# Kernel optimization log

Measured on AMD Instinct MI355X. Metric: run time of the kernel, lower is better.

## Reference

```python
import jax, jax.numpy as jnp
import numpy as np

D_MODEL = 1024
N_HEADS = 16
D_K = D_MODEL // N_HEADS
NEG = -1e9


def setup_inputs() -> dict:
    key = jax.random.key(0)
    ks = jax.random.split(key, 10)
    B, S = 4, 2048
    x = jax.random.normal(ks[0], (B, S, D_MODEL), dtype=jnp.float32)
    mask = jax.random.randint(ks[1], (B, S, S), 0, 2).astype(jnp.bool_)
    sc = 1.0 / np.sqrt(D_MODEL)
    Wq = jax.random.normal(ks[2], (D_MODEL, D_MODEL), dtype=jnp.float32) * sc
    bq = jnp.zeros((D_MODEL,), dtype=jnp.float32)
    Wk = jax.random.normal(ks[3], (D_MODEL, D_MODEL), dtype=jnp.float32) * sc
    bk = jnp.zeros((D_MODEL,), dtype=jnp.float32)
    Wv = jax.random.normal(ks[4], (D_MODEL, D_MODEL), dtype=jnp.float32) * sc
    bv = jnp.zeros((D_MODEL,), dtype=jnp.float32)
    Wo = jax.random.normal(ks[5], (D_MODEL, D_MODEL), dtype=jnp.float32) * sc
    bo = jnp.zeros((D_MODEL,), dtype=jnp.float32)
    return {"x": x, "mask": mask, "Wq": Wq, "bq": bq, "Wk": Wk, "bk": bk,
            "Wv": Wv, "bv": bv, "Wo": Wo, "bo": bo}


def _split_heads(t, B, S):
    # [B,S,d_model] -> [B,H,S,d_k]
    return t.reshape(B, S, N_HEADS, D_K).transpose(0, 2, 1, 3)


def reference(x, mask, Wq, bq, Wk, bk, Wv, bv, Wo, bo):
    B, S, _ = x.shape
    Q = _split_heads(x @ Wq + bq, B, S)
    K = _split_heads(x @ Wk + bk, B, S)
    V = _split_heads(x @ Wv + bv, B, S)
    scale = jnp.sqrt(jnp.float32(D_K))
    scores = jnp.einsum('bhqd,bhkd->bhqk', Q, K) / scale
    scores = jnp.where(mask[:, None, :, :], jnp.float32(NEG), scores)
    attn = jax.nn.softmax(scores, axis=-1)
    ctx = jnp.einsum('bhqk,bhkd->bhqd', attn, V)
    ctx = ctx.transpose(0, 2, 1, 3).reshape(B, S, D_MODEL)
    return ctx @ Wo + bo
```

## Files before the change

### kernel.cpp

```cpp
#include <hip/hip_runtime.h>

#define D_MODEL 1024
#define N_HEADS 16
#define D_K     64
#define BATCH   4
#define SEQ     2048
#define MROWS   (BATCH * SEQ)
#define QSCALE  0.18033688011112042f

typedef __bf16 bf16x8 __attribute__((ext_vector_type(8)));
typedef float  f32x4  __attribute__((ext_vector_type(4)));
typedef float  f32x16 __attribute__((ext_vector_type(16)));
typedef unsigned short ushort8 __attribute__((ext_vector_type(8)));
typedef unsigned short ushort4v __attribute__((ext_vector_type(4)));

#if __has_builtin(__builtin_amdgcn_exp2f)
#define EXP2F(x) __builtin_amdgcn_exp2f(x)
#else
#define EXP2F(x) exp2f(x)
#endif

#define CVT_PK_BF16(d, a, b) \
    asm("v_cvt_pk_bf16_f32 %0, %1, %2" : "=v"(d) : "v"(a), "v"(b))
#define PERMSWAP(a, b) \
    asm("v_permlane32_swap_b32 %0, %1" : "+v"(a), "+v"(b))
#define WAIT_VM(N) asm volatile("s_waitcnt vmcnt(" #N ")" ::: "memory")
#define CFENCE()   asm volatile("" ::: "memory")

__device__ inline unsigned short f2bf(float f) {
    union { float f; unsigned int u; } v; v.f = f;
    unsigned int u = v.u;
    unsigned int r = (u + 0x7fffu + ((u >> 16) & 1u)) >> 16;
    return (unsigned short)r;
}

__device__ inline void load_lds16(const void* g, void* l) {
    __builtin_amdgcn_global_load_lds(
        (const __attribute__((address_space(1))) unsigned int*)g,
        (__attribute__((address_space(3))) unsigned int*)l, 16, 0, 0);
}

__global__ __launch_bounds__(256) void wprep(const float* __restrict__ Wq,
                                             const float* __restrict__ Wk,
                                             const float* __restrict__ Wv,
                                             const float* __restrict__ Wo,
                                             unsigned short* __restrict__ wt) {
    __shared__ __align__(16) unsigned short t[64][65];
    int w  = blockIdx.z;
    const float* W = (w == 0) ? Wq : (w == 1) ? Wk : (w == 2) ? Wv : Wo;
    int k0 = blockIdx.x * 64, n0 = blockIdx.y * 64;
    int tid = threadIdx.x;
    int nl = tid & 63, kq = tid >> 6;
#pragma unroll
    for (int i = 0; i < 16; i++) {
        int kl = kq * 16 + i;
        t[kl][nl] = f2bf(W[(size_t)(k0 + kl) * D_MODEL + n0 + nl]);
    }
    __syncthreads();
    unsigned short* out = wt + (size_t)w * D_MODEL * D_MODEL;
#pragma unroll
    for (int p = 0; p < 2; p++) {
        int nrow = p * 32 + (tid >> 3);
        int c8   = (tid & 7) * 8;
        ushort8 o;
#pragma unroll
        for (int j = 0; j < 8; j++) o[j] = t[c8 + j][nrow];
        *reinterpret_cast<ushort8*>(out + (size_t)(n0 + nrow) * D_MODEL + k0 + c8) = o;
    }
}

__global__ __launch_bounds__(256) void xprep(const float4* __restrict__ x,
                                             unsigned short* __restrict__ xb) {
    int i = blockIdx.x * 256 + threadIdx.x;
    float4 v = x[i];
    ushort4v o;
    o[0] = f2bf(v.x); o[1] = f2bf(v.y); o[2] = f2bf(v.z); o[3] = f2bf(v.w);
    *reinterpret_cast<ushort4v*>(xb + (size_t)i * 4) = o;
}

__global__ __launch_bounds__(256) void mprep(const int* __restrict__ mask,
                                             unsigned long long* __restrict__ mb) {
    int row = blockIdx.x;
    int tid = threadIdx.x;
    int wv  = tid >> 6;
#pragma unroll
    for (int w = 0; w < 8; w++) {
        int col = w * 256 + tid;
        int mval = mask[(size_t)row * SEQ + col];
        unsigned long long bits = __ballot(mval != 0);
        if ((tid & 63) == 0) mb[(size_t)row * 32 + w * 4 + wv] = bits;
    }
}

__global__ __launch_bounds__(256) void qkv_gemm(const unsigned short* __restrict__ xb,
                                                const unsigned short* __restrict__ wt,
                                                const float* __restrict__ bq,
                                                const float* __restrict__ bk,
                                                const float* __restrict__ bvv,
                                                unsigned short* __restrict__ qb,
                                                unsigned short* __restrict__ kb,
                                                unsigned short* __restrict__ vt) {
    __shared__ __align__(16) unsigned short lds_a[128 * 32];
    __shared__ __align__(16) unsigned short lds_b[128 * 32];
    int tid = threadIdx.x;
    int wave = tid >> 6, lane = tid & 63;
    int c = lane & 15, g = lane >> 4;
    int wave_m = (wave & 1) * 64, wave_n = (wave >> 1) * 64;
    int wg = blockIdx.x;
    int swz = (wg & 7) * 192 + (wg >> 3);
    int nblk = (swz % 24) * 128, mblk = (swz / 24) * 128;

    int oct0 = wave * 128 + lane, oct1 = oct0 + 64;
    int ra0 = oct0 >> 2, ga0 = ((oct0 & 3) ^ (ra0 & 3)) * 8;
    int ra1 = oct1 >> 2, ga1 = ((oct1 & 3) ^ (ra1 & 3)) * 8;
    const unsigned short* pa0 = xb + (size_t)(mblk + ra0) * D_MODEL + ga0;
    const unsigned short* pa1 = xb + (size_t)(mblk + ra1) * D_MODEL + ga1;
    const unsigned short* pb0 = wt + (size_t)(nblk + ra0) * D_MODEL + ga0;
    const unsigned short* pb1 = wt + (size_t)(nblk + ra1) * D_MODEL + ga1;
    unsigned short* la0 = lds_a + wave * 1024;
    unsigned short* la1 = la0 + 512;
    unsigned short* lb0 = lds_b + wave * 1024;
    unsigned short* lb1 = lb0 + 512;

    int aoff[4], boff[4];
#pragma unroll
    for (int mi = 0; mi < 4; mi++) {
        int row = wave_m + mi * 16 + c;
        aoff[mi] = (row * 4 + (g ^ (row & 3))) * 16;
    }
#pragma unroll
    for (int ni = 0; ni < 4; ni++) {
        int row = wave_n + ni * 16 + c;
        boff[ni] = (row * 4 + (g ^ (row & 3))) * 16;
    }

    f32x4 acc[4][4];
#pragma unroll
    for (int mi = 0; mi < 4; mi++)
#pragma unroll
        for (int ni = 0; ni < 4; ni++) acc[mi][ni] = f32x4{0.f, 0.f, 0.f, 0.f};

    for (int k0 = 0; k0 < D_MODEL; k0 += 32) {
        load_lds16(pa0 + k0, la0);
        load_lds16(pa1 + k0, la1);
        load_lds16(pb0 + k0, lb0);
        load_lds16(pb1 + k0, lb1);
        __syncthreads();
        bf16x8 af[4], bfr[4];
#pragma unroll
        for (int mi = 0; mi < 4; mi++)
            af[mi] = *reinterpret_cast<const bf16x8*>(reinterpret_cast<const char*>(lds_a) + aoff[mi]);
#pragma unroll
        for (int ni = 0; ni < 4; ni++)
            bfr[ni] = *reinterpret_cast<const bf16x8*>(reinterpret_cast<const char*>(lds_b) + boff[ni]);
#pragma unroll
        for (int mi = 0; mi < 4; mi++)
#pragma unroll
            for (int ni = 0; ni < 4; ni++)
                acc[mi][ni] = __builtin_amdgcn_mfma_f32_16x16x32_bf16(af[mi], bfr[ni], acc[mi][ni], 0, 0, 0);
        __syncthreads();
    }

    int nb = nblk + wave_n;
    int wsel = nb >> 10;
    int h = (nb >> 6) & 15;
    int dk0 = nb & 63;
    int mglob = mblk + wave_m;
    int b = mglob >> 11;
    int s0 = mglob & (SEQ - 1);
    size_t bh = (size_t)(b * N_HEADS + h);
    const float* bias = (wsel == 0) ? bq : (wsel == 1) ? bk : bvv;
    int nn = nb & (D_MODEL - 1);
    float bval[4];
#pragma unroll
    for (int ni = 0; ni < 4; ni++) bval[ni] = bias[nn + ni * 16 + c];
    float oscale = (wsel == 0) ? QSCALE : 1.0f;

    if (wsel < 2) {
        unsigned short* outp = wsel ? kb : qb;
#pragma unroll
        for (int mi = 0; mi < 4; mi++)
#pragma unroll
            for (int ni = 0; ni < 4; ni++) {
                int dk = dk0 + ni * 16 + c;
#pragma unroll
                for (int r = 0; r < 4; r++) {
                    int s = s0 + mi * 16 + g * 4 + r;
                    outp[(bh * SEQ + s) * 64 + dk] = f2bf((acc[mi][ni][r] + bval[ni]) * oscale);
                }
            }
    } else {
#pragma unroll
        for (int mi = 0; mi < 4; mi++)
#pragma unroll
            for (int ni = 0; ni < 4; ni++) {
                int dk = dk0 + ni * 16 + c;
                int s = s0 + mi * 16 + g * 4;
                ushort4v o;
#pragma unroll
                for (int r = 0; r < 4; r++) o[r] = f2bf(acc[mi][ni][r] + bval[ni]);
                *reinterpret_cast<ushort4v*>(vt + (bh * 64 + dk) * SEQ + s) = o;
            }
    }
}

__global__ __launch_bounds__(128, 2) void attn(const unsigned short* __restrict__ qb,
                                               const unsigned short* __restrict__ kb,
                                               const unsigned short* __restrict__ vt,
                                               const unsigned long long* __restrict__ mb,
                                               unsigned short* __restrict__ ctx) {
    __shared__ __align__(16) unsigned char smem[32768];

    int tid = threadIdx.x;
    int wave = tid >> 6, lane = tid & 63;
    int q31 = lane & 31, hi = lane >> 5;
    int bid = blockIdx.x;
    int swz = (bid & 7) * 128 + (bid >> 3);
    int bh = swz >> 4;
    int q0 = (swz & 15) * 128 + wave * 64;
    int b = bh >> 4, h = bh & 15;
    const unsigned short* qbase = qb + (size_t)bh * SEQ * 64;
    const unsigned short* kbase = kb + (size_t)bh * SEQ * 64;
    const unsigned short* vbase = vt + (size_t)bh * 64 * SEQ;
    const unsigned long long* mp0 = mb + ((size_t)b * SEQ + q0 + q31) * 32;
    const unsigned long long* mp1 = mp0 + 1024;

    bf16x8 qf[2][4];
#pragma unroll
    for (int t = 0; t < 2; t++) {
        const unsigned short* qr = qbase + (size_t)(q0 + 32 * t + q31) * 64 + hi * 8;
#pragma unroll
        for (int c = 0; c < 4; c++)
            qf[t][c] = *reinterpret_cast<const bf16x8*>(qr + c * 16);
    }

    int srow = lane >> 3;
    int soct = (lane & 7) ^ srow;
    const unsigned short* ksrc[2];
    const unsigned short* vsrc[2];
    int stg[2];
#pragma unroll
    for (int i = 0; i < 2; i++) {
        int rbase = 16 * i + 8 * wave;
        ksrc[i] = kbase + (size_t)(rbase + srow) * 64 + soct * 8;
        vsrc[i] = vbase + (size_t)(rbase + srow) * SEQ + soct * 8;
        stg[i]  = rbase * 128;
    }
    const unsigned short* ksrc2[2];
    const unsigned short* vsrc2[2];
    int stg2[2];
#pragma unroll
    for (int i = 0; i < 2; i++) {
        int rbase = 32 + 16 * i + 8 * wave;
        ksrc2[i] = kbase + (size_t)(rbase + srow) * 64 + soct * 8;
        vsrc2[i] = vbase + (size_t)(rbase + srow) * SEQ + soct * 8;
        stg2[i]  = rbase * 128;
    }

    int kofs[2][4];
#pragma unroll
    for (int s = 0; s < 2; s++)
#pragma unroll
        for (int c = 0; c < 4; c++)
            kofs[s][c] = (32 * s + q31) * 128 + (((hi + 2 * c) ^ (q31 & 7)) * 16);

    float lsum[2] = {0.f, 0.f};
    f32x16 po[2][2];
#pragma unroll
    for (int i = 0; i < 16; i++) {
        po[0][0][i] = 0.f; po[0][1][i] = 0.f;
        po[1][0][i] = 0.f; po[1][1][i] = 0.f;
    }

    unsigned long long mnx0 = mp0[0], mnx1 = mp1[0];
    CFENCE();
#pragma unroll
    for (int i = 0; i < 2; i++) {
        load_lds16(ksrc[i], smem + stg[i]);
        load_lds16(vsrc[i], smem + 8192 + stg[i]);
        load_lds16(ksrc2[i], smem + stg2[i]);
        load_lds16(vsrc2[i], smem + 8192 + stg2[i]);
    }

    for (int it = 0; it < SEQ / 64; it++) {
        unsigned long long w64[2];
        w64[0] = mnx0; w64[1] = mnx1;
        int itn = (it + 1 < SEQ / 64) ? it + 1 : it;
        mnx0 = mp0[itn]; mnx1 = mp1[itn];
        CFENCE();
        unsigned char* bufn = smem + ((it + 1) & 1) * 16384;
#pragma unroll
        for (int i = 0; i < 2; i++) {
            load_lds16(ksrc[i] + itn * 4096, bufn + stg[i]);
            load_lds16(vsrc[i] + itn * 64,  bufn + 8192 + stg[i]);
            load_lds16(ksrc2[i] + itn * 4096, bufn + stg2[i]);
            load_lds16(vsrc2[i] + itn * 64,  bufn + 8192 + stg2[i]);
        }
        WAIT_VM(10);
        __builtin_amdgcn_s_barrier();
        CFENCE();

        const char* lkb = (const char*)(smem + (it & 1) * 16384);
        const char* lvb = lkb + 8192;

#pragma unroll
        for (int s = 0; s < 2; s++) {
            f32x16 sq[2];
#pragma unroll
            for (int i = 0; i < 16; i++) { sq[0][i] = 0.f; sq[1][i] = 0.f; }
#pragma unroll
            for (int c = 0; c < 4; c++) {
                bf16x8 kf = *reinterpret_cast<const bf16x8*>(lkb + kofs[s][c]);
                sq[0] = __builtin_amdgcn_mfma_f32_32x32x16_bf16(kf, qf[0][c], sq[0], 0, 0, 0);
                sq[1] = __builtin_amdgcn_mfma_f32_32x32x16_bf16(kf, qf[1][c], sq[1], 0, 0, 0);
            }
            union PF { uint4 u; bf16x8 v; };
            PF pf[2][2];
#pragma unroll
            for (int t = 0; t < 2; t++) {
                unsigned int wt_ = ~(unsigned int)(w64[t] >> (32 * s));
                float pm[16];
#pragma unroll
                for (int j = 0; j < 4; j++) {
                    unsigned int nj = wt_ >> (8 * j + 4 * hi);
#pragma unroll
                    for (int e = 0; e < 4; e++) {
                        float p = EXP2F(sq[t][4 * j + e]);
                        unsigned int m = (unsigned int)((int)(nj << (31 - e)) >> 31);
                        unsigned int pu = __float_as_uint(p) & m;
                        pm[4 * j + e] = __uint_as_float(pu);
                        lsum[t] += __uint_as_float(pu);
                    }
                }
                unsigned int w[8];
#pragma unroll
                for (int j = 0; j < 4; j++) {
                    CVT_PK_BF16(w[2 * j],     pm[4 * j + 0], pm[4 * j + 1]);
                    CVT_PK_BF16(w[2 * j + 1], pm[4 * j + 2], pm[4 * j + 3]);
                }
                PERMSWAP(w[0], w[2]); PERMSWAP(w[1], w[3]);
                PERMSWAP(w[4], w[6]); PERMSWAP(w[5], w[7]);
                pf[t][0].u = uint4{w[0], w[1], w[2], w[3]};
                pf[t][1].u = uint4{w[4], w[5], w[6], w[7]};
            }
#pragma unroll
            for (int cp = 0; cp < 2; cp++) {
                int c = 2 * s + cp;
#pragma unroll
                for (int so = 0; so < 2; so++) {
                    bf16x8 vf = *reinterpret_cast<const bf16x8*>(lvb + kofs[so][c]);
                    po[0][so] = __builtin_amdgcn_mfma_f32_32x32x16_bf16(vf, pf[0][cp].v, po[0][so], 0, 0, 0);
                    po[1][so] = __builtin_amdgcn_mfma_f32_32x32x16_bf16(vf, pf[1][cp].v, po[1][so], 0, 0, 0);
                }
            }
        }
        CFENCE();
        __builtin_amdgcn_s_barrier();
    }

    WAIT_VM(0);
    __builtin_amdgcn_s_barrier();

    float inv[2];
#pragma unroll
    for (int t = 0; t < 2; t++) {
        lsum[t] += __shfl_xor(lsum[t], 32);
        inv[t] = 1.f / lsum[t];
    }

    unsigned int* ob = (unsigned int*)(smem + wave * 8192);
    int csw = 4 * (q31 & 7);
#pragma unroll
    for (int t = 0; t < 2; t++) {
        unsigned int* obr = ob + (32 * t + q31) * 32;
#pragma unroll
        for (int so = 0; so < 2; so++)
#pragma unroll
            for (int j = 0; j < 4; j++) {
                unsigned int w0 = (unsigned int)f2bf(po[t][so][4 * j + 0] * inv[t])
                                | ((unsigned int)f2bf(po[t][so][4 * j + 1] * inv[t]) << 16);
                unsigned int w1 = (unsigned int)f2bf(po[t][so][4 * j + 2] * inv[t])
                                | ((unsigned int)f2bf(po[t][so][4 * j + 3] * inv[t]) << 16);
                int d = (16 * so + 4 * j + 2 * hi) ^ csw;
                uint2 u; u.x = w0; u.y = w1;
                *reinterpret_cast<uint2*>(obr + d) = u;
            }
    }
    __builtin_amdgcn_s_waitcnt(0);
    size_t crow = (size_t)b * SEQ + q0;
    int o = lane & 7, rl = lane >> 3;
#pragma unroll
    for (int i = 0; i < 8; i++) {
        int r = 8 * i + rl;
        uint4 v = *reinterpret_cast<const uint4*>(ob + r * 32 + 4 * (o ^ (r & 7)));
        *reinterpret_cast<uint4*>(ctx + (crow + r) * D_MODEL + h * 64 + o * 8) = v;
    }
}

__global__ __launch_bounds__(256) void oproj(const unsigned short* __restrict__ ctx,
                                             const unsigned short* __restrict__ wt,
                                             const float* __restrict__ bo,
                                             float* __restrict__ out) {
    __shared__ __align__(16) unsigned short lds_a[128 * 32];
    __shared__ __align__(16) unsigned short lds_b[128 * 32];
    int tid = threadIdx.x;
    int wave = tid >> 6, lane = tid & 63;
    int c = lane & 15, g = lane >> 4;
    int wave_m = (wave & 1) * 64, wave_n = (wave >> 1) * 64;
    int wg = blockIdx.x;
    int swz = (wg & 7) * 64 + (wg >> 3);
    int nblk = (swz & 7) * 128, mblk = (swz >> 3) * 128;
    const unsigned short* wo = wt + (size_t)3 * D_MODEL * D_MODEL;

    int oct0 = wave * 128 + lane, oct1 = oct0 + 64;
    int ra0 = oct0 >> 2, ga0 = ((oct0 & 3) ^ (ra0 & 3)) * 8;
    int ra1 = oct1 >> 2, ga1 = ((oct1 & 3) ^ (ra1 & 3)) * 8;
    const unsigned short* pa0 = ctx + (size_t)(mblk + ra0) * D_MODEL + ga0;
    const unsigned short* pa1 = ctx + (size_t)(mblk + ra1) * D_MODEL + ga1;
    const unsigned short* pb0 = wo + (size_t)(nblk + ra0) * D_MODEL + ga0;
    const unsigned short* pb1 = wo + (size_t)(nblk + ra1) * D_MODEL + ga1;
    unsigned short* la0 = lds_a + wave * 1024;
    unsigned short* la1 = la0 + 512;
    unsigned short* lb0 = lds_b + wave * 1024;
    unsigned short* lb1 = lb0 + 512;

    int aoff[4], boff[4];
#pragma unroll
    for (int mi = 0; mi < 4; mi++) {
        int row = wave_m + mi * 16 + c;
        aoff[mi] = (row * 4 + (g ^ (row & 3))) * 16;
    }
#pragma unroll
    for (int ni = 0; ni < 4; ni++) {
        int row = wave_n + ni * 16 + c;
        boff[ni] = (row * 4 + (g ^ (row & 3))) * 16;
    }

    f32x4 acc[4][4];
#pragma unroll
    for (int mi = 0; mi < 4; mi++)
#pragma unroll
        for (int ni = 0; ni < 4; ni++) acc[mi][ni] = f32x4{0.f, 0.f, 0.f, 0.f};

    for (int k0 = 0; k0 < D_MODEL; k0 += 32) {
        load_lds16(pa0 + k0, la0);
        load_lds16(pa1 + k0, la1);
        load_lds16(pb0 + k0, lb0);
        load_lds16(pb1 + k0, lb1);
        __syncthreads();
        bf16x8 af[4], bfr[4];
#pragma unroll
        for (int mi = 0; mi < 4; mi++)
            af[mi] = *reinterpret_cast<const bf16x8*>(reinterpret_cast<const char*>(lds_a) + aoff[mi]);
#pragma unroll
        for (int ni = 0; ni < 4; ni++)
            bfr[ni] = *reinterpret_cast<const bf16x8*>(reinterpret_cast<const char*>(lds_b) + boff[ni]);
#pragma unroll
        for (int mi = 0; mi < 4; mi++)
#pragma unroll
            for (int ni = 0; ni < 4; ni++)
                acc[mi][ni] = __builtin_amdgcn_mfma_f32_16x16x32_bf16(af[mi], bfr[ni], acc[mi][ni], 0, 0, 0);
        __syncthreads();
    }

    float bval[4];
#pragma unroll
    for (int ni = 0; ni < 4; ni++) bval[ni] = bo[nblk + wave_n + ni * 16 + c];
#pragma unroll
    for (int mi = 0; mi < 4; mi++)
#pragma unroll
        for (int ni = 0; ni < 4; ni++) {
            int n = nblk + wave_n + ni * 16 + c;
#pragma unroll
            for (int r = 0; r < 4; r++) {
                int m = mblk + wave_m + mi * 16 + g * 4 + r;
                out[(size_t)m * D_MODEL + n] = acc[mi][ni][r] + bval[ni];
            }
        }
}

extern "C" void kernel_launch(void* const* d_in, const int* in_sizes, int n_in,
                              void* d_out, int out_size, void* d_ws, size_t ws_size,
                              hipStream_t stream) {
    const float* x    = (const float*)d_in[0];
    const int*   mask = (const int*)d_in[1];
    const float* Wq = (const float*)d_in[2];
    const float* bq = (const float*)d_in[3];
    const float* Wk = (const float*)d_in[4];
    const float* bk = (const float*)d_in[5];
    const float* Wv = (const float*)d_in[6];
    const float* bv = (const float*)d_in[7];
    const float* Wo = (const float*)d_in[8];
    const float* bo = (const float*)d_in[9];
    float* out = (float*)d_out;

    char* ws = (char*)d_ws;
    const size_t MB = 1024 * 1024;
    unsigned short* wt  = (unsigned short*)(ws + 0 * MB);
    unsigned short* xb  = (unsigned short*)(ws + 8 * MB);
    unsigned short* qb  = (unsigned short*)(ws + 24 * MB);
    unsigned short* kb  = (unsigned short*)(ws + 40 * MB);
    unsigned short* vt  = (unsigned short*)(ws + 56 * MB);
    unsigned short* ctx = (unsigned short*)(ws + 72 * MB);
    unsigned long long* mb = (unsigned long long*)(ws + 88 * MB);

    wprep<<<dim3(16, 16, 4), 256, 0, stream>>>(Wq, Wk, Wv, Wo, wt);
    xprep<<<dim3(MROWS * D_MODEL / 4 / 256), 256, 0, stream>>>((const float4*)x, xb);
    mprep<<<dim3(MROWS), 256, 0, stream>>>(mask, mb);
    qkv_gemm<<<dim3(1536), 256, 0, stream>>>(xb, wt, bq, bk, bv, qb, kb, vt);
    attn<<<dim3(1024), 128, 0, stream>>>(qb, kb, vt, mb, ctx);
    oproj<<<dim3(512), 256, 0, stream>>>(ctx, wt, bo, out);
}
```

Measured before the change: 355.8 us.

## Split attention block into four waves of 32 query rows with MFMA priority

The attention kernel now runs 4 waves per block instead of 2. Each wave owns 32 query rows rather than 64, so it holds half the score and output accumulators, and each wave stages a quarter of the K/V tile. s_setprio is raised around the MFMA sections so the matrix work is favoured over the softmax/exp work of other waves. The aim is more waves in flight, better latency hiding and lower register pressure per wave. In exchange, each K fragment read from LDS now feeds only one MFMA instead of two, which increases LDS traffic per unit of compute.

```diff
diff --git a/kernel.cpp b/kernel.cpp
--- a/kernel.cpp
+++ b/kernel.cpp
@@ -204,11 +204,11 @@
     }
 }
 
-__global__ __launch_bounds__(128, 2) void attn(const unsigned short* __restrict__ qb,
-                                               const unsigned short* __restrict__ kb,
-                                               const unsigned short* __restrict__ vt,
-                                               const unsigned long long* __restrict__ mb,
-                                               unsigned short* __restrict__ ctx) {
+__global__ __launch_bounds__(256) void attn(const unsigned short* __restrict__ qb,
+                                            const unsigned short* __restrict__ kb,
+                                            const unsigned short* __restrict__ vt,
+                                            const unsigned long long* __restrict__ mb,
+                                            unsigned short* __restrict__ ctx) {
     __shared__ __align__(16) unsigned char smem[32768];
 
     int tid = threadIdx.x;
@@ -217,21 +217,20 @@
     int bid = blockIdx.x;
     int swz = (bid & 7) * 128 + (bid >> 3);
     int bh = swz >> 4;
-    int q0 = (swz & 15) * 128 + wave * 64;
+    int q0 = (swz & 15) * 128;
+    int qw = q0 + wave * 32;
     int b = bh >> 4, h = bh & 15;
     const unsigned short* qbase = qb + (size_t)bh * SEQ * 64;
     const unsigned short* kbase = kb + (size_t)bh * SEQ * 64;
     const unsigned short* vbase = vt + (size_t)bh * 64 * SEQ;
-    const unsigned long long* mp0 = mb + ((size_t)b * SEQ + q0 + q31) * 32;
-    const unsigned long long* mp1 = mp0 + 1024;
-
-    bf16x8 qf[2][4];
-#pragma unroll
-    for (int t = 0; t < 2; t++) {
-        const unsigned short* qr = qbase + (size_t)(q0 + 32 * t + q31) * 64 + hi * 8;
+    const unsigned long long* mp = mb + ((size_t)b * SEQ + qw + q31) * 32;
+
+    bf16x8 qf[4];
+    {
+        const unsigned short* qr = qbase + (size_t)(qw + q31) * 64 + hi * 8;
 #pragma unroll
         for (int c = 0; c < 4; c++)
-            qf[t][c] = *reinterpret_cast<const bf16x8*>(qr + c * 16);
+            qf[c] = *reinterpret_cast<const bf16x8*>(qr + c * 16);
     }
 
     int srow = lane >> 3;
@@ -241,21 +240,11 @@
     int stg[2];
 #pragma unroll
     for (int i = 0; i < 2; i++) {
-        int rbase = 16 * i + 8 * wave;
+        int rbase = 16 * wave + 8 * i;
         ksrc[i] = kbase + (size_t)(rbase + srow) * 64 + soct * 8;
         vsrc[i] = vbase + (size_t)(rbase + srow) * SEQ + soct * 8;
         stg[i]  = rbase * 128;
     }
-    const unsigned short* ksrc2[2];
-    const unsigned short* vsrc2[2];
-    int stg2[2];
-#pragma unroll
-    for (int i = 0; i < 2; i++) {
-        int rbase = 32 + 16 * i + 8 * wave;
-        ksrc2[i] = kbase + (size_t)(rbase + srow) * 64 + soct * 8;
-        vsrc2[i] = vbase + (size_t)(rbase + srow) * SEQ + soct * 8;
-        stg2[i]  = rbase * 128;
-    }
 
     int kofs[2][4];
 #pragma unroll
@@ -264,39 +253,31 @@
         for (int c = 0; c < 4; c++)
             kofs[s][c] = (32 * s + q31) * 128 + (((hi + 2 * c) ^ (q31 & 7)) * 16);
 
-    float lsum[2] = {0.f, 0.f};
-    f32x16 po[2][2];
-#pragma unroll
-    for (int i = 0; i < 16; i++) {
-        po[0][0][i] = 0.f; po[0][1][i] = 0.f;
-        po[1][0][i] = 0.f; po[1][1][i] = 0.f;
-    }
-
-    unsigned long long mnx0 = mp0[0], mnx1 = mp1[0];
+    float lsum = 0.f;
+    f32x16 po[2];
+#pragma unroll
+    for (int i = 0; i < 16; i++) { po[0][i] = 0.f; po[1][i] = 0.f; }
+
+    unsigned long long mnx = mp[0];
     CFENCE();
 #pragma unroll
     for (int i = 0; i < 2; i++) {
         load_lds16(ksrc[i], smem + stg[i]);
         load_lds16(vsrc[i], smem + 8192 + stg[i]);
-        load_lds16(ksrc2[i], smem + stg2[i]);
-        load_lds16(vsrc2[i], smem + 8192 + stg2[i]);
     }
 
     for (int it = 0; it < SEQ / 64; it++) {
-        unsigned long long w64[2];
-        w64[0] = mnx0; w64[1] = mnx1;
+        unsigned long long w64 = mnx;
         int itn = (it + 1 < SEQ / 64) ? it + 1 : it;
-        mnx0 = mp0[itn]; mnx1 = mp1[itn];
+        mnx = mp[itn];
         CFENCE();
         unsigned char* bufn = smem + ((it + 1) & 1) * 16384;
 #pragma unroll
         for (int i = 0; i < 2; i++) {
             load_lds16(ksrc[i] + itn * 4096, bufn + stg[i]);
             load_lds16(vsrc[i] + itn * 64,  bufn + 8192 + stg[i]);
-            load_lds16(ksrc2[i] + itn * 4096, bufn + stg2[i]);
-            load_lds16(vsrc2[i] + itn * 64,  bufn + 8192 + stg2[i]);
         }
-        WAIT_VM(10);
+        WAIT_VM(5);
         __builtin_amdgcn_s_barrier();
         CFENCE();
 
@@ -305,54 +286,53 @@
 
 #pragma unroll
         for (int s = 0; s < 2; s++) {
-            f32x16 sq[2];
-#pragma unroll
-            for (int i = 0; i < 16; i++) { sq[0][i] = 0.f; sq[1][i] = 0.f; }
+            f32x16 sq;
+#pragma unroll
+            for (int i = 0; i < 16; i++) sq[i] = 0.f;
+            __builtin_amdgcn_s_setprio(1);
 #pragma unroll
             for (int c = 0; c < 4; c++) {
                 bf16x8 kf = *reinterpret_cast<const bf16x8*>(lkb + kofs[s][c]);
-                sq[0] = __builtin_amdgcn_mfma_f32_32x32x16_bf16(kf, qf[0][c], sq[0], 0, 0, 0);
-                sq[1] = __builtin_amdgcn_mfma_f32_32x32x16_bf16(kf, qf[1][c], sq[1], 0, 0, 0);
-            }
+                sq = __builtin_amdgcn_mfma_f32_32x32x16_bf16(kf, qf[c], sq, 0, 0, 0);
+            }
+            __builtin_amdgcn_s_setprio(0);
             union PF { uint4 u; bf16x8 v; };
-            PF pf[2][2];
-#pragma unroll
-            for (int t = 0; t < 2; t++) {
-                unsigned int wt_ = ~(unsigned int)(w64[t] >> (32 * s));
-                float pm[16];
-#pragma unroll
-                for (int j = 0; j < 4; j++) {
-                    unsigned int nj = wt_ >> (8 * j + 4 * hi);
-#pragma unroll
-                    for (int e = 0; e < 4; e++) {
-                        float p = EXP2F(sq[t][4 * j + e]);
-                        unsigned int m = (unsigned int)((int)(nj << (31 - e)) >> 31);
-                        unsigned int pu = __float_as_uint(p) & m;
-                        pm[4 * j + e] = __uint_as_float(pu);
-                        lsum[t] += __uint_as_float(pu);
-                    }
+            PF pf[2];
+            unsigned int wt_ = ~(unsigned int)(w64 >> (32 * s));
+            float pm[16];
+#pragma unroll
+            for (int j = 0; j < 4; j++) {
+                unsigned int nj = wt_ >> (8 * j + 4 * hi);
+#pragma unroll
+                for (int e = 0; e < 4; e++) {
+                    float p = EXP2F(sq[4 * j + e]);
+                    unsigned int m = (unsigned int)((int)(nj << (31 - e)) >> 31);
+                    unsigned int pu = __float_as_uint(p) & m;
+                    pm[4 * j + e] = __uint_as_float(pu);
+                    lsum += __uint_as_float(pu);
                 }
-                unsigned int w[8];
-#pragma unroll
-                for (int j = 0; j < 4; j++) {
-                    CVT_PK_BF16(w[2 * j],     pm[4 * j + 0], pm[4 * j + 1]);
-                    CVT_PK_BF16(w[2 * j + 1], pm[4 * j + 2], pm[4 * j + 3]);
-                }
-                PERMSWAP(w[0], w[2]); PERMSWAP(w[1], w[3]);
-                PERMSWAP(w[4], w[6]); PERMSWAP(w[5], w[7]);
-                pf[t][0].u = uint4{w[0], w[1], w[2], w[3]};
-                pf[t][1].u = uint4{w[4], w[5], w[6], w[7]};
-            }
+            }
+            unsigned int w[8];
+#pragma unroll
+            for (int j = 0; j < 4; j++) {
+                CVT_PK_BF16(w[2 * j],     pm[4 * j + 0], pm[4 * j + 1]);
+                CVT_PK_BF16(w[2 * j + 1], pm[4 * j + 2], pm[4 * j + 3]);
+            }
+            PERMSWAP(w[0], w[2]); PERMSWAP(w[1], w[3]);
+            PERMSWAP(w[4], w[6]); PERMSWAP(w[5], w[7]);
+            pf[0].u = uint4{w[0], w[1], w[2], w[3]};
+            pf[1].u = uint4{w[4], w[5], w[6], w[7]};
+            __builtin_amdgcn_s_setprio(1);
 #pragma unroll
             for (int cp = 0; cp < 2; cp++) {
                 int c = 2 * s + cp;
 #pragma unroll
                 for (int so = 0; so < 2; so++) {
                     bf16x8 vf = *reinterpret_cast<const bf16x8*>(lvb + kofs[so][c]);
-                    po[0][so] = __builtin_amdgcn_mfma_f32_32x32x16_bf16(vf, pf[0][cp].v, po[0][so], 0, 0, 0);
-                    po[1][so] = __builtin_amdgcn_mfma_f32_32x32x16_bf16(vf, pf[1][cp].v, po[1][so], 0, 0, 0);
+                    po[so] = __builtin_amdgcn_mfma_f32_32x32x16_bf16(vf, pf[cp].v, po[so], 0, 0, 0);
                 }
             }
+            __builtin_amdgcn_s_setprio(0);
         }
         CFENCE();
         __builtin_amdgcn_s_barrier();
@@ -361,36 +341,29 @@
     WAIT_VM(0);
     __builtin_amdgcn_s_barrier();
 
-    float inv[2];
-#pragma unroll
-    for (int t = 0; t < 2; t++) {
-        lsum[t] += __shfl_xor(lsum[t], 32);
-        inv[t] = 1.f / lsum[t];
-    }
-
-    unsigned int* ob = (unsigned int*)(smem + wave * 8192);
+    lsum += __shfl_xor(lsum, 32);
+    float inv = 1.f / lsum;
+
+    unsigned int* ob = (unsigned int*)(smem + wave * 4096);
     int csw = 4 * (q31 & 7);
-#pragma unroll
-    for (int t = 0; t < 2; t++) {
-        unsigned int* obr = ob + (32 * t + q31) * 32;
-#pragma unroll
-        for (int so = 0; so < 2; so++)
-#pragma unroll
-            for (int j = 0; j < 4; j++) {
-                unsigned int w0 = (unsigned int)f2bf(po[t][so][4 * j + 0] * inv[t])
-                                | ((unsigned int)f2bf(po[t][so][4 * j + 1] * inv[t]) << 16);
-                unsigned int w1 = (unsigned int)f2bf(po[t][so][4 * j + 2] * inv[t])
-                                | ((unsigned int)f2bf(po[t][so][4 * j + 3] * inv[t]) << 16);
-                int d = (16 * so + 4 * j + 2 * hi) ^ csw;
-                uint2 u; u.x = w0; u.y = w1;
-                *reinterpret_cast<uint2*>(obr + d) = u;
-            }
-    }
+    unsigned int* obr = ob + q31 * 32;
+#pragma unroll
+    for (int so = 0; so < 2; so++)
+#pragma unroll
+        for (int j = 0; j < 4; j++) {
+            unsigned int w0 = (unsigned int)f2bf(po[so][4 * j + 0] * inv)
+                            | ((unsigned int)f2bf(po[so][4 * j + 1] * inv) << 16);
+            unsigned int w1 = (unsigned int)f2bf(po[so][4 * j + 2] * inv)
+                            | ((unsigned int)f2bf(po[so][4 * j + 3] * inv) << 16);
+            int d = (16 * so + 4 * j + 2 * hi) ^ csw;
+            uint2 u; u.x = w0; u.y = w1;
+            *reinterpret_cast<uint2*>(obr + d) = u;
+        }
     __builtin_amdgcn_s_waitcnt(0);
-    size_t crow = (size_t)b * SEQ + q0;
+    size_t crow = (size_t)b * SEQ + qw;
     int o = lane & 7, rl = lane >> 3;
 #pragma unroll
-    for (int i = 0; i < 8; i++) {
+    for (int i = 0; i < 4; i++) {
         int r = 8 * i + rl;
         uint4 v = *reinterpret_cast<const uint4*>(ob + r * 32 + 4 * (o ^ (r & 7)));
         *reinterpret_cast<uint4*>(ctx + (crow + r) * D_MODEL + h * 64 + o * 8) = v;
@@ -508,6 +481,6 @@
     xprep<<<dim3(MROWS * D_MODEL / 4 / 256), 256, 0, stream>>>((const float4*)x, xb);
     mprep<<<dim3(MROWS), 256, 0, stream>>>(mask, mb);
     qkv_gemm<<<dim3(1536), 256, 0, stream>>>(xb, wt, bq, bk, bv, qb, kb, vt);
-    attn<<<dim3(1024), 128, 0, stream>>>(qb, kb, vt, mb, ctx);
+    attn<<<dim3(1024), 256, 0, stream>>>(qb, kb, vt, mb, ctx);
     oproj<<<dim3(512), 256, 0, stream>>>(ctx, wt, bo, out);
 }
```

After: 370.8 us. +4.2%, slower.

## Double-buffer LDS tiles in QKV and output-projection GEMM main loops

Applied to the files above, without the earlier changes.

Both GEMM kernels now keep two LDS buffers per operand and issue the global-to-LDS loads for the next K-slice before computing on the current one, waiting with a partial vmcnt instead of a full sync. This is meant to hide global memory latency behind the MFMA work. LDS use per block doubles, which may cut occupancy, and the last iteration issues a redundant reload.

```diff
diff --git a/kernel.cpp b/kernel.cpp
--- a/kernel.cpp
+++ b/kernel.cpp
@@ -100,8 +100,8 @@
                                                 unsigned short* __restrict__ qb,
                                                 unsigned short* __restrict__ kb,
                                                 unsigned short* __restrict__ vt) {
-    __shared__ __align__(16) unsigned short lds_a[128 * 32];
-    __shared__ __align__(16) unsigned short lds_b[128 * 32];
+    __shared__ __align__(16) unsigned short lds_a[2][128 * 32];
+    __shared__ __align__(16) unsigned short lds_b[2][128 * 32];
     int tid = threadIdx.x;
     int wave = tid >> 6, lane = tid & 63;
     int c = lane & 15, g = lane >> 4;
@@ -117,10 +117,7 @@
     const unsigned short* pa1 = xb + (size_t)(mblk + ra1) * D_MODEL + ga1;
     const unsigned short* pb0 = wt + (size_t)(nblk + ra0) * D_MODEL + ga0;
     const unsigned short* pb1 = wt + (size_t)(nblk + ra1) * D_MODEL + ga1;
-    unsigned short* la0 = lds_a + wave * 1024;
-    unsigned short* la1 = la0 + 512;
-    unsigned short* lb0 = lds_b + wave * 1024;
-    unsigned short* lb1 = lb0 + 512;
+    int wofs = wave * 1024;
 
     int aoff[4], boff[4];
 #pragma unroll
@@ -140,26 +137,39 @@
 #pragma unroll
         for (int ni = 0; ni < 4; ni++) acc[mi][ni] = f32x4{0.f, 0.f, 0.f, 0.f};
 
-    for (int k0 = 0; k0 < D_MODEL; k0 += 32) {
-        load_lds16(pa0 + k0, la0);
-        load_lds16(pa1 + k0, la1);
-        load_lds16(pb0 + k0, lb0);
-        load_lds16(pb1 + k0, lb1);
-        __syncthreads();
+    load_lds16(pa0, &lds_a[0][wofs]);
+    load_lds16(pa1, &lds_a[0][wofs + 512]);
+    load_lds16(pb0, &lds_b[0][wofs]);
+    load_lds16(pb1, &lds_b[0][wofs + 512]);
+
+    for (int i = 0; i < 32; i++) {
+        int kn = (i + 1 < 32) ? (i + 1) * 32 : i * 32;
+        int bn = (i + 1) & 1;
+        load_lds16(pa0 + kn, &lds_a[bn][wofs]);
+        load_lds16(pa1 + kn, &lds_a[bn][wofs + 512]);
+        load_lds16(pb0 + kn, &lds_b[bn][wofs]);
+        load_lds16(pb1 + kn, &lds_b[bn][wofs + 512]);
+        WAIT_VM(4);
+        __builtin_amdgcn_s_barrier();
+        CFENCE();
+        const char* ba = (const char*)lds_a[i & 1];
+        const char* bbp = (const char*)lds_b[i & 1];
         bf16x8 af[4], bfr[4];
 #pragma unroll
         for (int mi = 0; mi < 4; mi++)
-            af[mi] = *reinterpret_cast<const bf16x8*>(reinterpret_cast<const char*>(lds_a) + aoff[mi]);
+            af[mi] = *reinterpret_cast<const bf16x8*>(ba + aoff[mi]);
 #pragma unroll
         for (int ni = 0; ni < 4; ni++)
-            bfr[ni] = *reinterpret_cast<const bf16x8*>(reinterpret_cast<const char*>(lds_b) + boff[ni]);
+            bfr[ni] = *reinterpret_cast<const bf16x8*>(bbp + boff[ni]);
 #pragma unroll
         for (int mi = 0; mi < 4; mi++)
 #pragma unroll
             for (int ni = 0; ni < 4; ni++)
                 acc[mi][ni] = __builtin_amdgcn_mfma_f32_16x16x32_bf16(af[mi], bfr[ni], acc[mi][ni], 0, 0, 0);
-        __syncthreads();
-    }
+        CFENCE();
+        __builtin_amdgcn_s_barrier();
+    }
+    WAIT_VM(0);
 
     int nb = nblk + wave_n;
     int wsel = nb >> 10;
@@ -401,8 +411,8 @@
                                              const unsigned short* __restrict__ wt,
                                              const float* __restrict__ bo,
                                              float* __restrict__ out) {
-    __shared__ __align__(16) unsigned short lds_a[128 * 32];
-    __shared__ __align__(16) unsigned short lds_b[128 * 32];
+    __shared__ __align__(16) unsigned short lds_a[2][128 * 32];
+    __shared__ __align__(16) unsigned short lds_b[2][128 * 32];
     int tid = threadIdx.x;
     int wave = tid >> 6, lane = tid & 63;
     int c = lane & 15, g = lane >> 4;
@@ -419,10 +429,7 @@
     const unsigned short* pa1 = ctx + (size_t)(mblk + ra1) * D_MODEL + ga1;
     const unsigned short* pb0 = wo + (size_t)(nblk + ra0) * D_MODEL + ga0;
     const unsigned short* pb1 = wo + (size_t)(nblk + ra1) * D_MODEL + ga1;
-    unsigned short* la0 = lds_a + wave * 1024;
-    unsigned short* la1 = la0 + 512;
-    unsigned short* lb0 = lds_b + wave * 1024;
-    unsigned short* lb1 = lb0 + 512;
+    int wofs = wave * 1024;
 
     int aoff[4], boff[4];
 #pragma unroll
@@ -442,26 +449,39 @@
 #pragma unroll
         for (int ni = 0; ni < 4; ni++) acc[mi][ni] = f32x4{0.f, 0.f, 0.f, 0.f};
 
-    for (int k0 = 0; k0 < D_MODEL; k0 += 32) {
-        load_lds16(pa0 + k0, la0);
-        load_lds16(pa1 + k0, la1);
-        load_lds16(pb0 + k0, lb0);
-        load_lds16(pb1 + k0, lb1);
-        __syncthreads();
+    load_lds16(pa0, &lds_a[0][wofs]);
+    load_lds16(pa1, &lds_a[0][wofs + 512]);
+    load_lds16(pb0, &lds_b[0][wofs]);
+    load_lds16(pb1, &lds_b[0][wofs + 512]);
+
+    for (int i = 0; i < 32; i++) {
+        int kn = (i + 1 < 32) ? (i + 1) * 32 : i * 32;
+        int bn = (i + 1) & 1;
+        load_lds16(pa0 + kn, &lds_a[bn][wofs]);
+        load_lds16(pa1 + kn, &lds_a[bn][wofs + 512]);
+        load_lds16(pb0 + kn, &lds_b[bn][wofs]);
+        load_lds16(pb1 + kn, &lds_b[bn][wofs + 512]);
+        WAIT_VM(4);
+        __builtin_amdgcn_s_barrier();
+        CFENCE();
+        const char* ba = (const char*)lds_a[i & 1];
+        const char* bbp = (const char*)lds_b[i & 1];
         bf16x8 af[4], bfr[4];
 #pragma unroll
         for (int mi = 0; mi < 4; mi++)
-            af[mi] = *reinterpret_cast<const bf16x8*>(reinterpret_cast<const char*>(lds_a) + aoff[mi]);
+            af[mi] = *reinterpret_cast<const bf16x8*>(ba + aoff[mi]);
 #pragma unroll
         for (int ni = 0; ni < 4; ni++)
-            bfr[ni] = *reinterpret_cast<const bf16x8*>(reinterpret_cast<const char*>(lds_b) + boff[ni]);
+            bfr[ni] = *reinterpret_cast<const bf16x8*>(bbp + boff[ni]);
 #pragma unroll
         for (int mi = 0; mi < 4; mi++)
 #pragma unroll
             for (int ni = 0; ni < 4; ni++)
                 acc[mi][ni] = __builtin_amdgcn_mfma_f32_16x16x32_bf16(af[mi], bfr[ni], acc[mi][ni], 0, 0, 0);
-        __syncthreads();
-    }
+        CFENCE();
+        __builtin_amdgcn_s_barrier();
+    }
+    WAIT_VM(0);
 
     float bval[4];
 #pragma unroll
```

New measurement: 366.9 us. +3.1%, slower.
